# Kernel optimization log

Hardware: AMD Instinct MI355X
Metric: run time of the kernel (lower is better)

The kernel has to match this reference:

```python
import jax, jax.numpy as jnp
import numpy as np

B, N, D, R = 4, 2048, 1024, 64
LN_EPS = 1e-5


def setup_inputs() -> dict:
    key = jax.random.key(0)
    k_x, k_m, k_u, k_v = jax.random.split(key, 4)
    x = jax.random.normal(k_x, (B, N, D), dtype=jnp.float32)
    mask = jax.random.uniform(k_m, (B, N, R), dtype=jnp.float32)
    # xavier-style init for low-rank bases U_max, V_max: (d_model, R_max)
    scale = jnp.sqrt(2.0 / (D + R)).astype(jnp.float32)
    U = jax.random.normal(k_u, (D, R), dtype=jnp.float32) * scale
    V = jax.random.normal(k_v, (D, R), dtype=jnp.float32) * scale
    gamma = jnp.ones((D,), dtype=jnp.float32)
    beta = jnp.zeros((D,), dtype=jnp.float32)
    return {"x": x, "mask": mask, "U": U, "V": V, "gamma": gamma, "beta": beta}


def _layernorm(y, gamma, beta):
    mu = jnp.mean(y, axis=-1, keepdims=True)
    var = jnp.mean(jnp.square(y - mu), axis=-1, keepdims=True)
    return (y - mu) * jax.lax.rsqrt(var + LN_EPS) * gamma + beta


def reference(x, mask, U, V, gamma, beta):
    # Q/K: low-rank projections gated by per-token continuous mask
    Q = jnp.einsum('bnd,dr->bnr', x, U) * mask            # (B, N, R)
    K = jnp.einsum('bnd,dr->bnr', x, V) * mask            # (B, N, R)
    # effective rank per query token, clamped at 1
    r_eff = jnp.maximum(jnp.sum(mask, axis=-1, keepdims=True), 1.0)  # (B, N, 1)
    scores = jnp.einsum('bqr,bkr->bqk', Q, K) / jnp.sqrt(r_eff)      # (B, N, N)
    A = jax.nn.softmax(scores, axis=-1)
    delta = jnp.einsum('bqk,bkd->bqd', A, x)              # (B, N, D)
    # backbone is identity: out = LN(x + delta)
    return _layernorm(x + delta, gamma, beta)
```

## Files before the change

kernel.cpp:

```cpp
#include <hip/hip_runtime.h>

#define Bb 4
#define Nn 2048
#define Dd 1024
#define Rr 64
#define LN_EPS 1e-5f

typedef unsigned short u16;
typedef short bf16x8 __attribute__((ext_vector_type(8)));
typedef float f32x4 __attribute__((ext_vector_type(4)));

__device__ __forceinline__ u16 f2bf(float f) {
  unsigned u = __float_as_uint(f);
  u += 0x7FFFu + ((u >> 16) & 1u);
  return (u16)(u >> 16);
}

__device__ __forceinline__ void g2l16(u16* l, const u16* g) {
  __builtin_amdgcn_global_load_lds(
      (const __attribute__((address_space(1))) unsigned int*)g,
      (__attribute__((address_space(3))) unsigned int*)l, 16, 0, 0);
}

__global__ __launch_bounds__(256) void prep_x(const float* __restrict__ x,
                                              u16* __restrict__ xt) {
  __shared__ float tile[64][65];
  const int b = blockIdx.z;
  const int n0 = blockIdx.x * 64;
  const int d0 = blockIdx.y * 64;
  const int t = threadIdx.x;
  const int c = t & 63, r4 = t >> 6;
#pragma unroll
  for (int rr = 0; rr < 16; rr++) {
    int row = rr * 4 + r4;
    tile[row][c] = x[(size_t)(b * Nn + n0 + row) * Dd + d0 + c];
  }
  __syncthreads();
#pragma unroll
  for (int rr = 0; rr < 16; rr++) {
    int dd = rr * 4 + r4;
    xt[(size_t)(b * Dd + d0 + dd) * Nn + n0 + c] = f2bf(tile[c][dd]);
  }
}

__global__ __launch_bounds__(256) void prep_small(const float* __restrict__ U,
    const float* __restrict__ V, const float* __restrict__ mask,
    u16* __restrict__ uvt, float* __restrict__ qs) {
  if (blockIdx.x < 32) {
    __shared__ float tile[64][65];
    const int which = blockIdx.x >> 4;
    const int d0 = (blockIdx.x & 15) * 64;
    const float* src = which ? V : U;
    const int t = threadIdx.x, c = t & 63, r4 = t >> 6;
#pragma unroll
    for (int rr = 0; rr < 16; rr++) {
      int row = rr * 4 + r4;
      tile[row][c] = src[(size_t)(d0 + row) * Rr + c];
    }
    __syncthreads();
#pragma unroll
    for (int rr = 0; rr < 16; rr++) {
      int r = rr * 4 + r4;
      uvt[(size_t)(which * 64 + r) * Dd + d0 + c] = f2bf(tile[c][r]);
    }
  } else {
    const int row = (blockIdx.x - 32) * 4 + (threadIdx.x >> 6);
    const int lane = threadIdx.x & 63;
    float v = mask[(size_t)row * Rr + lane];
#pragma unroll
    for (int off = 32; off; off >>= 1) v += __shfl_xor(v, off);
    if (lane == 0) qs[row] = rsqrtf(fmaxf(v, 1.0f));
  }
}

__global__ __launch_bounds__(256) void proj_qk(const float* __restrict__ x,
    const float* __restrict__ mask, const u16* __restrict__ uvt,
    u16* __restrict__ Qo, u16* __restrict__ Ko) {
  const int t = threadIdx.x;
  const int w = t >> 6, l = t & 63, quad = l >> 4, l16 = l & 15;
  const int g0 = blockIdx.x * 32;
  f32x4 acc[2][2];
#pragma unroll
  for (int i = 0; i < 2; i++)
#pragma unroll
    for (int j = 0; j < 2; j++) acc[i][j] = (f32x4){0.f, 0.f, 0.f, 0.f};
  for (int k0 = 0; k0 < Dd; k0 += 32) {
    bf16x8 a[2];
#pragma unroll
    for (int mt = 0; mt < 2; mt++) {
      const float4* px = (const float4*)&x[(size_t)(g0 + mt * 16 + l16) * Dd + k0 + quad * 8];
      float4 x0 = px[0], x1 = px[1];
      bf16x8 av;
      av[0] = (short)f2bf(x0.x); av[1] = (short)f2bf(x0.y);
      av[2] = (short)f2bf(x0.z); av[3] = (short)f2bf(x0.w);
      av[4] = (short)f2bf(x1.x); av[5] = (short)f2bf(x1.y);
      av[6] = (short)f2bf(x1.z); av[7] = (short)f2bf(x1.w);
      a[mt] = av;
    }
    bf16x8 bfr[2];
#pragma unroll
    for (int i = 0; i < 2; i++) {
      int col = (w * 2 + i) * 16 + l16;
      bfr[i] = *(const bf16x8*)&uvt[(size_t)col * Dd + k0 + quad * 8];
    }
#pragma unroll
    for (int mt = 0; mt < 2; mt++)
#pragma unroll
      for (int i = 0; i < 2; i++)
        acc[mt][i] = __builtin_amdgcn_mfma_f32_16x16x32_bf16(a[mt], bfr[i], acc[mt][i], 0, 0, 0);
  }
#pragma unroll
  for (int mt = 0; mt < 2; mt++)
#pragma unroll
    for (int i = 0; i < 2; i++) {
      int col = (w * 2 + i) * 16 + l16;
      int r_ = col & 63;
#pragma unroll
      for (int r = 0; r < 4; r++) {
        int row = g0 + mt * 16 + quad * 4 + r;
        float v = acc[mt][i][r] * mask[(size_t)row * Rr + r_];
        u16 bv = f2bf(v);
        if (col < 64) Qo[(size_t)row * Rr + r_] = bv;
        else          Ko[(size_t)row * Rr + r_] = bv;
      }
    }
}

__global__ __launch_bounds__(512, 2) void score_softmax(
    const u16* __restrict__ Qm, const u16* __restrict__ Km,
    const float* __restrict__ qs, u16* __restrict__ Pw,
    float* __restrict__ linv_g) {
  __shared__ float red[32][8];
  __shared__ float mfin[32];
  const int t = threadIdx.x;
  const int w = t >> 6, l = t & 63, quad = l >> 4, l16 = l & 15;
  const int id = blockIdx.x;
  const int xcd = id & 7;
  const int b = xcd >> 1;
  const int q0 = (((id >> 3) << 1) | (xcd & 1)) * 32;
  bf16x8 qf[2][2];
#pragma unroll
  for (int mt = 0; mt < 2; mt++)
#pragma unroll
    for (int ks = 0; ks < 2; ks++)
      qf[mt][ks] = *(const bf16x8*)&Qm[(size_t)(b * Nn + q0 + mt * 16 + l16) * Rr + ks * 32 + quad * 8];
  f32x4 acc[2][16];
#pragma unroll
  for (int mt = 0; mt < 2; mt++)
#pragma unroll
    for (int nt = 0; nt < 16; nt++) acc[mt][nt] = (f32x4){0.f, 0.f, 0.f, 0.f};
#pragma unroll
  for (int nt = 0; nt < 16; nt++) {
#pragma unroll
    for (int ks = 0; ks < 2; ks++) {
      bf16x8 kf = *(const bf16x8*)&Km[(size_t)(b * Nn + w * 256 + nt * 16 + l16) * Rr + ks * 32 + quad * 8];
#pragma unroll
      for (int mt = 0; mt < 2; mt++)
        acc[mt][nt] = __builtin_amdgcn_mfma_f32_16x16x32_bf16(qf[mt][ks], kf, acc[mt][nt], 0, 0, 0);
    }
  }
  float sc[2][4];
#pragma unroll
  for (int mt = 0; mt < 2; mt++)
#pragma unroll
    for (int r = 0; r < 4; r++)
      sc[mt][r] = qs[(size_t)b * Nn + q0 + mt * 16 + quad * 4 + r];
#pragma unroll
  for (int mt = 0; mt < 2; mt++)
#pragma unroll
    for (int nt = 0; nt < 16; nt++)
#pragma unroll
      for (int r = 0; r < 4; r++) acc[mt][nt][r] *= sc[mt][r];
  float vmax[2][4];
#pragma unroll
  for (int mt = 0; mt < 2; mt++)
#pragma unroll
    for (int r = 0; r < 4; r++) {
      float m = -1e30f;
#pragma unroll
      for (int nt = 0; nt < 16; nt++) m = fmaxf(m, acc[mt][nt][r]);
#pragma unroll
      for (int off = 1; off < 16; off <<= 1) m = fmaxf(m, __shfl_xor(m, off));
      vmax[mt][r] = m;
    }
  if (l16 == 0) {
#pragma unroll
    for (int mt = 0; mt < 2; mt++)
#pragma unroll
      for (int r = 0; r < 4; r++) red[mt * 16 + quad * 4 + r][w] = vmax[mt][r];
  }
  __syncthreads();
  if (t < 32) {
    float m = -1e30f;
#pragma unroll
    for (int i = 0; i < 8; i++) m = fmaxf(m, red[t][i]);
    mfin[t] = m;
  }
  __syncthreads();
  float rowm[2][4], vsum[2][4];
#pragma unroll
  for (int mt = 0; mt < 2; mt++)
#pragma unroll
    for (int r = 0; r < 4; r++) {
      rowm[mt][r] = mfin[mt * 16 + quad * 4 + r];
      vsum[mt][r] = 0.f;
    }
#pragma unroll
  for (int mt = 0; mt < 2; mt++)
#pragma unroll
    for (int nt = 0; nt < 16; nt++)
#pragma unroll
      for (int r = 0; r < 4; r++) {
        float p = __expf(acc[mt][nt][r] - rowm[mt][r]);
        acc[mt][nt][r] = p;
        vsum[mt][r] += p;
      }
#pragma unroll
  for (int mt = 0; mt < 2; mt++)
#pragma unroll
    for (int r = 0; r < 4; r++) {
#pragma unroll
      for (int off = 1; off < 16; off <<= 1) vsum[mt][r] += __shfl_xor(vsum[mt][r], off);
    }
  __syncthreads();
  if (l16 == 0) {
#pragma unroll
    for (int mt = 0; mt < 2; mt++)
#pragma unroll
      for (int r = 0; r < 4; r++) red[mt * 16 + quad * 4 + r][w] = vsum[mt][r];
  }
  __syncthreads();
  if (t < 32) {
    float s = 0.f;
#pragma unroll
    for (int i = 0; i < 8; i++) s += red[t][i];
    linv_g[(size_t)b * Nn + q0 + t] = 1.f / s;
  }
#pragma unroll
  for (int mt = 0; mt < 2; mt++)
#pragma unroll
    for (int nt = 0; nt < 16; nt++) {
      const size_t base = ((size_t)(b * Nn + q0 + mt * 16 + quad * 4)) * Nn + w * 256 + nt * 16 + l16;
#pragma unroll
      for (int r = 0; r < 4; r++)
        Pw[base + (size_t)r * Nn] = f2bf(acc[mt][nt][r]);
    }
}

__global__ __launch_bounds__(256, 2) void pv_gemm(
    const u16* __restrict__ Pw, const u16* __restrict__ xt,
    const float* __restrict__ x, const float* __restrict__ linv_g,
    float* __restrict__ y) {
  __shared__ u16 As[128 * 64];
  __shared__ u16 Bs[128 * 64];
  const int t = threadIdx.x;
  const int w = t >> 6, l = t & 63, quad = l >> 4, l16 = l & 15;
  const int id = blockIdx.x;
  const int xcd = id & 7;
  const int b = xcd >> 1;
  const int nh = xcd & 1;
  const int rest = id >> 3;
  const int m0 = (rest & 15) * 128;
  const int n0 = (nh * 4 + (rest >> 4)) * 128;
  const int srow = w * 32 + (l >> 3);
  const int skoff = (((l & 7) ^ ((l >> 3) & 7)) * 8);
  f32x4 acc[4][4];
#pragma unroll
  for (int i = 0; i < 4; i++)
#pragma unroll
    for (int j = 0; j < 4; j++) acc[i][j] = (f32x4){0.f, 0.f, 0.f, 0.f};
  const int wm = w & 1, wn = w >> 1;
  const int sw = (l16 & 7);
  for (int k0 = 0; k0 < Nn; k0 += 64) {
    __syncthreads();
#pragma unroll
    for (int c = 0; c < 4; c++) {
      int row = srow + c * 8;
      g2l16(&As[(w * 32 + c * 8) * 64],
            &Pw[((size_t)(b * Nn + m0 + row)) * Nn + k0 + skoff]);
      g2l16(&Bs[(w * 32 + c * 8) * 64],
            &xt[((size_t)(b * Dd + n0 + row)) * Nn + k0 + skoff]);
    }
    __syncthreads();
#pragma unroll
    for (int ks = 0; ks < 2; ks++) {
      const int slot = ((ks * 4 + quad) ^ sw) * 8;
      bf16x8 af[4], bf_[4];
#pragma unroll
      for (int mt = 0; mt < 4; mt++)
        af[mt] = *(const bf16x8*)&As[(wm * 64 + mt * 16 + l16) * 64 + slot];
#pragma unroll
      for (int nt = 0; nt < 4; nt++)
        bf_[nt] = *(const bf16x8*)&Bs[(wn * 64 + nt * 16 + l16) * 64 + slot];
#pragma unroll
      for (int mt = 0; mt < 4; mt++)
#pragma unroll
        for (int nt = 0; nt < 4; nt++)
          acc[mt][nt] = __builtin_amdgcn_mfma_f32_16x16x32_bf16(af[mt], bf_[nt], acc[mt][nt], 0, 0, 0);
    }
  }
  float li[4][4];
#pragma unroll
  for (int mt = 0; mt < 4; mt++)
#pragma unroll
    for (int r = 0; r < 4; r++)
      li[mt][r] = linv_g[(size_t)b * Nn + m0 + wm * 64 + mt * 16 + quad * 4 + r];
#pragma unroll
  for (int mt = 0; mt < 4; mt++)
#pragma unroll
    for (int nt = 0; nt < 4; nt++) {
      const int nn = n0 + wn * 64 + nt * 16 + l16;
#pragma unroll
      for (int r = 0; r < 4; r++) {
        const int m = m0 + wm * 64 + mt * 16 + quad * 4 + r;
        const size_t off = ((size_t)(b * Nn + m)) * Dd + nn;
        y[off] = x[off] + li[mt][r] * acc[mt][nt][r];
      }
    }
}

__global__ __launch_bounds__(256) void ln_k(float* __restrict__ y,
    const float* __restrict__ gamma, const float* __restrict__ beta) {
  __shared__ float rs[4], rq[4];
  const int row = blockIdx.x;
  const int t = threadIdx.x;
  float* p = y + (size_t)row * Dd;
  float4 v = ((const float4*)p)[t];
  float s = v.x + v.y + v.z + v.w;
  float q = v.x * v.x + v.y * v.y + v.z * v.z + v.w * v.w;
#pragma unroll
  for (int off = 32; off; off >>= 1) {
    s += __shfl_xor(s, off);
    q += __shfl_xor(q, off);
  }
  if ((t & 63) == 0) { rs[t >> 6] = s; rq[t >> 6] = q; }
  __syncthreads();
  float S = rs[0] + rs[1] + rs[2] + rs[3];
  float Q2 = rq[0] + rq[1] + rq[2] + rq[3];
  float mu = S * (1.f / Dd);
  float var = Q2 * (1.f / Dd) - mu * mu;
  float rstd = rsqrtf(var + LN_EPS);
  float4 g = ((const float4*)gamma)[t];
  float4 be = ((const float4*)beta)[t];
  v.x = (v.x - mu) * rstd * g.x + be.x;
  v.y = (v.y - mu) * rstd * g.y + be.y;
  v.z = (v.z - mu) * rstd * g.z + be.z;
  v.w = (v.w - mu) * rstd * g.w + be.w;
  ((float4*)p)[t] = v;
}

extern "C" void kernel_launch(void* const* d_in, const int* in_sizes, int n_in,
                              void* d_out, int out_size, void* d_ws, size_t ws_size,
                              hipStream_t stream) {
  const float* x     = (const float*)d_in[0];
  const float* mask  = (const float*)d_in[1];
  const float* U     = (const float*)d_in[2];
  const float* V     = (const float*)d_in[3];
  const float* gamma = (const float*)d_in[4];
  const float* beta  = (const float*)d_in[5];
  float* out = (float*)d_out;
  char* ws = (char*)d_ws;
  u16*   xt   = (u16*)ws;
  u16*   Qw   = (u16*)(ws + (size_t)(16 << 20));
  u16*   Kw   = (u16*)(ws + (size_t)(17 << 20));
  u16*   uvt  = (u16*)(ws + (size_t)(18 << 20));
  float* qsb  = (float*)(ws + (size_t)(18 << 20) + (256 << 10));
  float* linv = (float*)(ws + (size_t)(18 << 20) + (288 << 10));
  u16*   Pw   = (u16*)(ws + (size_t)(19 << 20));

  prep_x       <<<dim3(Nn / 64, Dd / 64, Bb), 256, 0, stream>>>(x, xt);
  prep_small   <<<32 + (Bb * Nn) / 4, 256, 0, stream>>>(U, V, mask, uvt, qsb);
  proj_qk      <<<(Bb * Nn) / 32, 256, 0, stream>>>(x, mask, uvt, Qw, Kw);
  score_softmax<<<Bb * (Nn / 32), 512, 0, stream>>>(Qw, Kw, qsb, Pw, linv);
  pv_gemm      <<<Bb * (Nn / 128) * (Dd / 128), 256, 0, stream>>>(Pw, xt, x, linv, out);
  ln_k         <<<Bb * Nn, 256, 0, stream>>>(out, gamma, beta);
}
```

Before: 189.7 us.

## Triple-buffer PV GEMM with 256x128 tiles and interleaved async loads

The PV GEMM now uses 512-thread blocks on 256x128 output tiles and a three-stage LDS ring. Global-to-LDS loads for tile k+2 are issued in chunks between MFMA phases, gated by explicit vmcnt waits and s_setprio, so memory latency overlaps with compute instead of the load/sync/compute pattern. prep_x also packs two bf16 values per 32-bit store in the transpose. LDS use grows to about 144KB per block, which may limit occupancy and relies on hand-tuned waitcnt values being correct.

Result: slower. 197.9 us (+4.4%).

```diff
diff --git a/kernel.cpp b/kernel.cpp
--- a/kernel.cpp
+++ b/kernel.cpp
@@ -20,6 +20,12 @@
   __builtin_amdgcn_global_load_lds(
       (const __attribute__((address_space(1))) unsigned int*)g,
       (__attribute__((address_space(3))) unsigned int*)l, 16, 0, 0);
+}
+
+__device__ __forceinline__ void fence_barrier() {
+  asm volatile("" ::: "memory");
+  __builtin_amdgcn_s_barrier();
+  asm volatile("" ::: "memory");
 }
 
 __global__ __launch_bounds__(256) void prep_x(const float* __restrict__ x,
@@ -36,10 +42,13 @@
     tile[row][c] = x[(size_t)(b * Nn + n0 + row) * Dd + d0 + c];
   }
   __syncthreads();
-#pragma unroll
-  for (int rr = 0; rr < 16; rr++) {
-    int dd = rr * 4 + r4;
-    xt[(size_t)(b * Dd + d0 + dd) * Nn + n0 + c] = f2bf(tile[c][dd]);
+  const int c2 = t & 31, r8 = t >> 5;
+#pragma unroll
+  for (int rr = 0; rr < 8; rr++) {
+    int dd = rr * 8 + r8;
+    unsigned lo = f2bf(tile[2 * c2][dd]);
+    unsigned hi = f2bf(tile[2 * c2 + 1][dd]);
+    *(unsigned*)&xt[(size_t)(b * Dd + d0 + dd) * Nn + n0 + 2 * c2] = lo | (hi << 16);
   }
 }
 
@@ -247,12 +256,12 @@
     }
 }
 
-__global__ __launch_bounds__(256, 2) void pv_gemm(
+__global__ __launch_bounds__(512, 2) void pv_gemm(
     const u16* __restrict__ Pw, const u16* __restrict__ xt,
     const float* __restrict__ x, const float* __restrict__ linv_g,
     float* __restrict__ y) {
-  __shared__ u16 As[128 * 64];
-  __shared__ u16 Bs[128 * 64];
+  __shared__ u16 As[3][256 * 64];
+  __shared__ u16 Bs[3][128 * 64];
   const int t = threadIdx.x;
   const int w = t >> 6, l = t & 63, quad = l >> 4, l16 = l & 15;
   const int id = blockIdx.x;
@@ -260,45 +269,113 @@
   const int b = xcd >> 1;
   const int nh = xcd & 1;
   const int rest = id >> 3;
-  const int m0 = (rest & 15) * 128;
-  const int n0 = (nh * 4 + (rest >> 4)) * 128;
-  const int srow = w * 32 + (l >> 3);
-  const int skoff = (((l & 7) ^ ((l >> 3) & 7)) * 8);
+  const int m0 = (rest >> 2) * 256;
+  const int n0 = (nh * 4 + (rest & 3)) * 128;
+  const int lrow = l >> 3;
+  const int skoff = ((l & 7) ^ lrow) * 8;
+  const size_t gA = (size_t)(b * Nn + m0 + w * 8 + lrow) * Nn + skoff;
+  const size_t gB = (size_t)(b * Dd + n0 + w * 8 + lrow) * Nn + skoff;
+  const int wm = w >> 1, wn = w & 1;
+  const int sw = l16 & 7;
   f32x4 acc[4][4];
 #pragma unroll
   for (int i = 0; i < 4; i++)
 #pragma unroll
     for (int j = 0; j < 4; j++) acc[i][j] = (f32x4){0.f, 0.f, 0.f, 0.f};
-  const int wm = w & 1, wn = w >> 1;
-  const int sw = (l16 & 7);
-  for (int k0 = 0; k0 < Nn; k0 += 64) {
-    __syncthreads();
-#pragma unroll
-    for (int c = 0; c < 4; c++) {
-      int row = srow + c * 8;
-      g2l16(&As[(w * 32 + c * 8) * 64],
-            &Pw[((size_t)(b * Nn + m0 + row)) * Nn + k0 + skoff]);
-      g2l16(&Bs[(w * 32 + c * 8) * 64],
-            &xt[((size_t)(b * Dd + n0 + row)) * Nn + k0 + skoff]);
-    }
-    __syncthreads();
-#pragma unroll
-    for (int ks = 0; ks < 2; ks++) {
-      const int slot = ((ks * 4 + quad) ^ sw) * 8;
-      bf16x8 af[4], bf_[4];
-#pragma unroll
-      for (int mt = 0; mt < 4; mt++)
-        af[mt] = *(const bf16x8*)&As[(wm * 64 + mt * 16 + l16) * 64 + slot];
-#pragma unroll
-      for (int nt = 0; nt < 4; nt++)
-        bf_[nt] = *(const bf16x8*)&Bs[(wn * 64 + nt * 16 + l16) * 64 + slot];
-#pragma unroll
-      for (int mt = 0; mt < 4; mt++)
-#pragma unroll
-        for (int nt = 0; nt < 4; nt++)
-          acc[mt][nt] = __builtin_amdgcn_mfma_f32_16x16x32_bf16(af[mt], bf_[nt], acc[mt][nt], 0, 0, 0);
-    }
-  }
+
+#define STA(bf, j, k0) g2l16(&As[bf][((j) * 64 + w * 8) * 64], \
+                             &Pw[gA + (size_t)(j) * 64 * Nn + (size_t)(k0)])
+#define STB(bf, j, k0) g2l16(&Bs[bf][((j) * 64 + w * 8) * 64], \
+                             &xt[gB + (size_t)(j) * 64 * Nn + (size_t)(k0)])
+
+#pragma unroll
+  for (int j = 0; j < 4; j++) STA(0, j, 0);
+  STB(0, 0, 0);
+  STB(0, 1, 0);
+#pragma unroll
+  for (int j = 0; j < 4; j++) STA(1, j, 64);
+  STB(1, 0, 64);
+  STB(1, 1, 64);
+
+  int bufc = 0;
+  for (int kt = 0; kt < Nn / 64; kt++) {
+    if (kt == Nn / 64 - 1) asm volatile("s_waitcnt vmcnt(0)" ::: "memory");
+    else                   asm volatile("s_waitcnt vmcnt(6)" ::: "memory");
+    __builtin_amdgcn_s_barrier();
+    asm volatile("" ::: "memory");
+    const int bufs = (bufc == 0) ? 2 : bufc - 1;
+    const int k2 = (kt + 2) * 64;
+    const bool st = kt < Nn / 64 - 2;
+    bf16x8 af[4], bfr[4];
+    {
+      const int slot = (quad ^ sw) * 8;
+#pragma unroll
+      for (int mt = 0; mt < 4; mt++)
+        af[mt] = *(const bf16x8*)&As[bufc][(wm * 64 + mt * 16 + l16) * 64 + slot];
+#pragma unroll
+      for (int nt = 0; nt < 2; nt++)
+        bfr[nt] = *(const bf16x8*)&Bs[bufc][(wn * 64 + nt * 16 + l16) * 64 + slot];
+      if (st) { STA(bufs, 0, k2); STA(bufs, 1, k2); }
+      __builtin_amdgcn_s_setprio(1);
+#pragma unroll
+      for (int mt = 0; mt < 4; mt++)
+#pragma unroll
+        for (int nt = 0; nt < 2; nt++)
+          acc[mt][nt] = __builtin_amdgcn_mfma_f32_16x16x32_bf16(af[mt], bfr[nt], acc[mt][nt], 0, 0, 0);
+      __builtin_amdgcn_s_setprio(0);
+      fence_barrier();
+    }
+    {
+      const int slot = (quad ^ sw) * 8;
+#pragma unroll
+      for (int nt = 2; nt < 4; nt++)
+        bfr[nt] = *(const bf16x8*)&Bs[bufc][(wn * 64 + nt * 16 + l16) * 64 + slot];
+      if (st) { STA(bufs, 2, k2); STA(bufs, 3, k2); }
+      __builtin_amdgcn_s_setprio(1);
+#pragma unroll
+      for (int mt = 0; mt < 4; mt++)
+#pragma unroll
+        for (int nt = 2; nt < 4; nt++)
+          acc[mt][nt] = __builtin_amdgcn_mfma_f32_16x16x32_bf16(af[mt], bfr[nt], acc[mt][nt], 0, 0, 0);
+      __builtin_amdgcn_s_setprio(0);
+      fence_barrier();
+    }
+    {
+      const int slot = ((4 + quad) ^ sw) * 8;
+#pragma unroll
+      for (int mt = 0; mt < 4; mt++)
+        af[mt] = *(const bf16x8*)&As[bufc][(wm * 64 + mt * 16 + l16) * 64 + slot];
+#pragma unroll
+      for (int nt = 0; nt < 2; nt++)
+        bfr[nt] = *(const bf16x8*)&Bs[bufc][(wn * 64 + nt * 16 + l16) * 64 + slot];
+      if (st) STB(bufs, 0, k2);
+      __builtin_amdgcn_s_setprio(1);
+#pragma unroll
+      for (int mt = 0; mt < 4; mt++)
+#pragma unroll
+        for (int nt = 0; nt < 2; nt++)
+          acc[mt][nt] = __builtin_amdgcn_mfma_f32_16x16x32_bf16(af[mt], bfr[nt], acc[mt][nt], 0, 0, 0);
+      __builtin_amdgcn_s_setprio(0);
+      fence_barrier();
+    }
+    {
+      const int slot = ((4 + quad) ^ sw) * 8;
+#pragma unroll
+      for (int nt = 2; nt < 4; nt++)
+        bfr[nt] = *(const bf16x8*)&Bs[bufc][(wn * 64 + nt * 16 + l16) * 64 + slot];
+      if (st) STB(bufs, 1, k2);
+      __builtin_amdgcn_s_setprio(1);
+#pragma unroll
+      for (int mt = 0; mt < 4; mt++)
+#pragma unroll
+        for (int nt = 2; nt < 4; nt++)
+          acc[mt][nt] = __builtin_amdgcn_mfma_f32_16x16x32_bf16(af[mt], bfr[nt], acc[mt][nt], 0, 0, 0);
+      __builtin_amdgcn_s_setprio(0);
+    }
+    bufc = (bufc == 2) ? 0 : bufc + 1;
+  }
+#undef STA
+#undef STB
   float li[4][4];
 #pragma unroll
   for (int mt = 0; mt < 4; mt++)
@@ -372,6 +449,6 @@
   prep_small   <<<32 + (Bb * Nn) / 4, 256, 0, stream>>>(U, V, mask, uvt, qsb);
   proj_qk      <<<(Bb * Nn) / 32, 256, 0, stream>>>(x, mask, uvt, Qw, Kw);
   score_softmax<<<Bb * (Nn / 32), 512, 0, stream>>>(Qw, Kw, qsb, Pw, linv);
-  pv_gemm      <<<Bb * (Nn / 128) * (Dd / 128), 256, 0, stream>>>(Pw, xt, x, linv, out);
+  pv_gemm      <<<Bb * (Nn / 256) * (Dd / 128), 512, 0, stream>>>(Pw, xt, x, linv, out);
   ln_k         <<<Bb * Nn, 256, 0, stream>>>(out, gamma, beta);
 }
```
